# Kernel tuning notes

Measured on AMD Instinct MI355X. Metric: run time of the kernel, lower is better.

The kernel has to match this reference:

```python
import jax, jax.numpy as jnp
import numpy as np

B, T, S, D, VOCAB = 16, 64, 128, 512, 32000


def setup_inputs():
    key = jax.random.key(0)
    ks = jax.random.split(key, 20)
    w = lambda i, shape: jax.random.normal(ks[i], shape, dtype=jnp.float32) * 0.05
    return {
        'words': jax.random.randint(ks[0], (B, T), 0, VOCAB),
        'encoder_output': jax.random.normal(ks[1], (B, S, D), dtype=jnp.float32),
        'pre_h': jax.random.normal(ks[2], (B, D), dtype=jnp.float32),
        'cell': jax.random.normal(ks[3], (B, D), dtype=jnp.float32),
        'emb': w(4, (VOCAB, D)),
        'W_ih': w(5, (4 * D, D)), 'W_hh': w(6, (4 * D, D)),
        'b_ih': w(7, (4 * D,)), 'b_hh': w(8, (4 * D,)),
        'Wh_w': w(9, (D, D)),
        'Ws_w': w(10, (D, D)), 'Ws_b': w(11, (D,)),
        'vt_w': w(12, (D,)),
        'V_w': w(13, (D, 2 * D)), 'V_b': w(14, (D,)),
        'Vp_w': w(15, (VOCAB, D)), 'Vp_b': w(16, (VOCAB,)),
    }


def lstm(xs, h0, c0, W_ih, W_hh, b_ih, b_hh):
    # xs: [T, B, D]; PyTorch LSTM gate order: i, f, g, o
    def step(carry, x_t):
        h, c = carry
        g = x_t @ W_ih.T + b_ih + h @ W_hh.T + b_hh
        i, f, gg, o = jnp.split(g, 4, axis=-1)
        c = jax.nn.sigmoid(f) * c + jax.nn.sigmoid(i) * jnp.tanh(gg)
        h = jax.nn.sigmoid(o) * jnp.tanh(c)
        return (h, c), h
    _, hs = jax.lax.scan(step, (h0, c0), xs)
    return hs


def reference(words, encoder_output, pre_h, cell, emb, W_ih, W_hh, b_ih, b_hh,
              Wh_w, Ws_w, Ws_b, vt_w, V_w, V_b, Vp_w, Vp_b):
    x = emb[words]                                   # [B, T, D]
    hs = lstm(x.transpose(1, 0, 2), pre_h, cell, W_ih, W_hh, b_ih, b_hh)
    out = hs.transpose(1, 0, 2)                      # [B, T, D] decoder states
    wh = encoder_output @ Wh_w.T                     # [B, S, D]
    ws = out @ Ws_w.T + Ws_b                         # [B, T, D]
    # Bahdanau additive attention scores e[b,s,t] = v_t . tanh(wh[b,s] + ws[b,t])
    e = jnp.einsum('bstd,d->bst', jnp.tanh(wh[:, :, None, :] + ws[:, None, :, :]), vt_w)
    a = jax.nn.softmax(e, axis=1)                    # softmax over source positions
    context = jnp.einsum('bst,bsd->btd', a, encoder_output)
    cat = jnp.concatenate([context, out], axis=-1)   # [B, T, 2D]
    return (cat @ V_w.T + V_b) @ Vp_w.T + Vp_b       # [B, T, VOCAB]
```

## Files before the change

### kernel.cpp

```cpp
#include <hip/hip_runtime.h>

#define DEV __device__ __forceinline__

typedef float f32x4 __attribute__((ext_vector_type(4)));
typedef short s16x8 __attribute__((ext_vector_type(8)));
typedef unsigned short u16;
typedef u16 u16x4 __attribute__((ext_vector_type(4)));
typedef u16 u16x8 __attribute__((ext_vector_type(8)));
typedef unsigned int u32x4 __attribute__((ext_vector_type(4)));

constexpr int Bb = 16, Tt = 64, Ss = 128, Dd = 512, Vv = 32000, FD = 2048;

DEV u16 f2bf(float x) {
  unsigned u = __builtin_bit_cast(unsigned, x);
  u = u + 0x7fffu + ((u >> 16) & 1u);
  return (u16)(u >> 16);
}
DEV float bf2f(u16 h) { unsigned u = ((unsigned)h) << 16; return __builtin_bit_cast(float, u); }
DEV float sigm(float x) { return 1.f / (1.f + __expf(-x)); }
DEV float ftanh(float x) {
  x = fminf(15.f, fmaxf(-15.f, x));
  float e = __expf(2.f * x);
  return (e - 1.f) / (e + 1.f);
}

DEV void cvt_plain_one(const float* __restrict__ in, u16* __restrict__ out, int i) {
  float4 v = reinterpret_cast<const float4*>(in)[i];
  u16x4 o;
  o.x = f2bf(v.x); o.y = f2bf(v.y); o.z = f2bf(v.z); o.w = f2bf(v.w);
  reinterpret_cast<u16x4*>(out)[i] = o;
}

DEV void cvt_split_one(const float* __restrict__ in, u16* __restrict__ hi,
                       u16* __restrict__ lo, int i) {
  float4 v = reinterpret_cast<const float4*>(in)[i];
  u16x4 oh, ol;
  float vv[4] = {v.x, v.y, v.z, v.w};
#pragma unroll
  for (int j = 0; j < 4; ++j) {
    u16 h = f2bf(vv[j]);
    oh[j] = h;
    ol[j] = f2bf(vv[j] - bf2f(h));
  }
  reinterpret_cast<u16x4*>(hi)[i] = oh;
  reinterpret_cast<u16x4*>(lo)[i] = ol;
}

__global__ void k_cvt_pre(const float* __restrict__ Wih, u16* __restrict__ Wih_bf, int n0,
                          const float* __restrict__ enc, u16* __restrict__ ench,
                          u16* __restrict__ encl, int n1,
                          const float* __restrict__ Whw, u16* __restrict__ whh,
                          u16* __restrict__ whl, int n2) {
  int total = n0 + n1 + n2;
  int i = blockIdx.x * blockDim.x + threadIdx.x;
  int st = gridDim.x * blockDim.x;
  for (; i < total; i += st) {
    if (i < n0) cvt_plain_one(Wih, Wih_bf, i);
    else if (i < n0 + n1) cvt_split_one(enc, ench, encl, i - n0);
    else cvt_split_one(Whw, whh, whl, i - n0 - n1);
  }
}

__global__ void k_prep(const int* __restrict__ words, const float* __restrict__ emb,
                       u16* __restrict__ xb,
                       const float* __restrict__ pre, unsigned* __restrict__ hp0,
                       const float* __restrict__ bi, const float* __restrict__ bh,
                       float* __restrict__ bsum) {
  int blk = blockIdx.x, tid = threadIdx.x;
  if (blk < Bb * Tt) {
    int row = words[blk];
    int d = tid * 2;
    float2 v = *reinterpret_cast<const float2*>(&emb[(size_t)row * Dd + d]);
    xb[(size_t)blk * Dd + d] = f2bf(v.x);
    xb[(size_t)blk * Dd + d + 1] = f2bf(v.y);
  } else if (blk < Bb * Tt + 32) {
    int i = (blk - Bb * Tt) * 256 + tid;
    float v = pre[i];
    u16 h = f2bf(v);
    u16 l = f2bf(v - bf2f(h));
    hp0[i] = (unsigned)h | ((unsigned)l << 16);
  } else {
    int i = (blk - Bb * Tt - 32) * 256 + tid;
    bsum[i] = bi[i] + bh[i];
  }
}

template <bool BIAS, bool OUTBF, int TERMS>
DEV void gemm_body(u16* ls, int tile, int tid,
                   const u16* __restrict__ A, const u16* __restrict__ Al,
                   const u16* __restrict__ Bm, const u16* __restrict__ Bl,
                   float* __restrict__ Cf, u16* __restrict__ Cb,
                   const float* __restrict__ bias, int M, int N, int K) {
  u16* lsA = ls;
  u16* lsB = ls + 128 * 32;
  u16* lsAl = ls + 2 * 128 * 32;
  u16* lsBl = ls + 3 * 128 * 32;
  const int mt = M >> 7;
  const int tm = (tile % mt) << 7;
  const int tn = (tile / mt) << 7;
  const int wave = tid >> 6, lane = tid & 63;
  const int wr = wave >> 1, wc = wave & 1;
  f32x4 acc[4][4];
#pragma unroll
  for (int i = 0; i < 4; ++i)
#pragma unroll
    for (int j = 0; j < 4; ++j) acc[i][j] = (f32x4){0.f, 0.f, 0.f, 0.f};

  const int lrow = lane >> 2;
  const int lk = (lane & 3) << 3;
  const int fr = lane & 15, fk = (lane >> 4) << 3;

  for (int k0 = 0; k0 < K; k0 += 32) {
#pragma unroll
    for (int r = 0; r < 2; ++r) {
      int rowA = r * 64 + wave * 16;
      size_t goffA = (size_t)(tm + rowA + lrow) * K + k0 + lk;
      size_t goffB = (size_t)(tn + rowA + lrow) * K + k0 + lk;
      __builtin_amdgcn_global_load_lds((const __attribute__((address_space(1))) void*)(A + goffA),
                                       (__attribute__((address_space(3))) void*)&lsA[rowA * 32],
                                       16, 0, 0);
      __builtin_amdgcn_global_load_lds((const __attribute__((address_space(1))) void*)(Bm + goffB),
                                       (__attribute__((address_space(3))) void*)&lsB[rowA * 32],
                                       16, 0, 0);
      if constexpr (TERMS == 3) {
        __builtin_amdgcn_global_load_lds((const __attribute__((address_space(1))) void*)(Al + goffA),
                                         (__attribute__((address_space(3))) void*)&lsAl[rowA * 32],
                                         16, 0, 0);
        __builtin_amdgcn_global_load_lds((const __attribute__((address_space(1))) void*)(Bl + goffB),
                                         (__attribute__((address_space(3))) void*)&lsBl[rowA * 32],
                                         16, 0, 0);
      }
    }
    __syncthreads();
    s16x8 av[4], bv[4];
#pragma unroll
    for (int mi = 0; mi < 4; ++mi)
      av[mi] = *reinterpret_cast<const s16x8*>(&lsA[(wr * 64 + mi * 16 + fr) * 32 + fk]);
#pragma unroll
    for (int ni = 0; ni < 4; ++ni)
      bv[ni] = *reinterpret_cast<const s16x8*>(&lsB[(wc * 64 + ni * 16 + fr) * 32 + fk]);
    if constexpr (TERMS == 3) {
      s16x8 avl[4], bvl[4];
#pragma unroll
      for (int mi = 0; mi < 4; ++mi)
        avl[mi] = *reinterpret_cast<const s16x8*>(&lsAl[(wr * 64 + mi * 16 + fr) * 32 + fk]);
#pragma unroll
      for (int ni = 0; ni < 4; ++ni)
        bvl[ni] = *reinterpret_cast<const s16x8*>(&lsBl[(wc * 64 + ni * 16 + fr) * 32 + fk]);
#pragma unroll
      for (int mi = 0; mi < 4; ++mi)
#pragma unroll
        for (int ni = 0; ni < 4; ++ni) {
          acc[mi][ni] = __builtin_amdgcn_mfma_f32_16x16x32_bf16(av[mi], bv[ni], acc[mi][ni], 0, 0, 0);
          acc[mi][ni] = __builtin_amdgcn_mfma_f32_16x16x32_bf16(av[mi], bvl[ni], acc[mi][ni], 0, 0, 0);
          acc[mi][ni] = __builtin_amdgcn_mfma_f32_16x16x32_bf16(avl[mi], bv[ni], acc[mi][ni], 0, 0, 0);
        }
    } else {
#pragma unroll
      for (int mi = 0; mi < 4; ++mi)
#pragma unroll
        for (int ni = 0; ni < 4; ++ni)
          acc[mi][ni] = __builtin_amdgcn_mfma_f32_16x16x32_bf16(av[mi], bv[ni], acc[mi][ni], 0, 0, 0);
    }
    __syncthreads();
  }

  const int fm = (lane >> 4) << 2;
#pragma unroll
  for (int ni = 0; ni < 4; ++ni) {
    int col = tn + wc * 64 + ni * 16 + fr;
    float badd = 0.f;
    if constexpr (BIAS) badd = bias[col];
#pragma unroll
    for (int mi = 0; mi < 4; ++mi) {
#pragma unroll
      for (int r = 0; r < 4; ++r) {
        int row = tm + wr * 64 + mi * 16 + fm + r;
        size_t idx = (size_t)row * N + col;
        float v = acc[mi][ni][r] + badd;
        if constexpr (OUTBF) Cb[idx] = f2bf(v);
        else Cf[idx] = v;
      }
    }
  }
}

template <bool BIAS, bool OUTBF, int TERMS>
__global__ __launch_bounds__(256) void k_gemm(const u16* __restrict__ A,
                                              const u16* __restrict__ Al,
                                              const u16* __restrict__ Bm,
                                              const u16* __restrict__ Bl,
                                              float* __restrict__ Cf, u16* __restrict__ Cb,
                                              const float* __restrict__ bias,
                                              int M, int N, int K) {
  __shared__ u16 ls[4 * 128 * 32];
  gemm_body<BIAS, OUTBF, TERMS>(ls, blockIdx.x, threadIdx.x, A, Al, Bm, Bl, Cf, Cb, bias, M, N, K);
}

DEV void lstm_body(int w, int tid, float* gls,
                   const float* __restrict__ xg, const float* __restrict__ Whh,
                   const float* __restrict__ cell, unsigned* __restrict__ hpack,
                   u16* __restrict__ out_hi, u16* __restrict__ out_lo,
                   int* __restrict__ flags) {
  const int gi = tid >> 6, lane = tid & 63;
  const int ds0 = w << 4;
  float (*g_lds)[16][16] = (float(*)[16][16])gls;

  const int fr = lane & 15;
  const int fkb = (lane >> 4) << 3;

  s16x8 whi[16], wlo[16];
  {
    const float* wrow = Whh + (size_t)(gi * Dd + ds0 + fr) * Dd;
#pragma unroll
    for (int kc = 0; kc < 16; ++kc) {
      int k = kc * 32 + fkb;
      float4 a = *reinterpret_cast<const float4*>(&wrow[k]);
      float4 b = *reinterpret_cast<const float4*>(&wrow[k + 4]);
      float vv[8] = {a.x, a.y, a.z, a.w, b.x, b.y, b.z, b.w};
#pragma unroll
      for (int j = 0; j < 8; ++j) {
        u16 h = f2bf(vv[j]);
        whi[kc][j] = (short)h;
        wlo[kc][j] = (short)f2bf(vv[j] - bf2f(h));
      }
    }
  }

  const int ub = tid >> 4, ud = tid & 15;
  float c = cell[(size_t)ub * Dd + ds0 + ud];

  for (int t = 0; t < Tt; ++t) {
    float xgv[4];
#pragma unroll
    for (int r = 0; r < 4; ++r) {
      int bb = ((lane >> 4) << 2) + r;
      xgv[r] = xg[(size_t)(bb * Tt + t) * FD + gi * Dd + ds0 + fr];
    }
#pragma unroll
    for (int r = 0; r < 4; ++r) asm volatile("" ::"v"(xgv[r]));

    if (t > 0) {
      if (gi == 0) {
        if (lane < 32 && lane != w) {
          while (__hip_atomic_load(&flags[lane * 32], __ATOMIC_RELAXED,
                                   __HIP_MEMORY_SCOPE_AGENT) < t) {}
          while (__hip_atomic_load(&flags[lane * 32], __ATOMIC_ACQUIRE,
                                   __HIP_MEMORY_SCOPE_AGENT) < t) {}
        }
        __builtin_amdgcn_sched_barrier(0);
      }
      __syncthreads();
    }

    const unsigned* hp = hpack + (size_t)t * (Bb * Dd) + (size_t)fr * Dd;
    f32x4 a0 = (f32x4){0.f, 0.f, 0.f, 0.f};
    f32x4 a1 = a0, a2 = a0;
#pragma unroll
    for (int kc = 0; kc < 16; ++kc) {
      int k = kc * 32 + fkb;
      u32x4 u0 = *reinterpret_cast<const u32x4*>(&hp[k]);
      u32x4 u1 = *reinterpret_cast<const u32x4*>(&hp[k + 4]);
      s16x8 ahi, alo;
#pragma unroll
      for (int j = 0; j < 4; ++j) {
        ahi[j] = (short)(u0[j] & 0xffffu); alo[j] = (short)(u0[j] >> 16);
        ahi[4 + j] = (short)(u1[j] & 0xffffu); alo[4 + j] = (short)(u1[j] >> 16);
      }
      a0 = __builtin_amdgcn_mfma_f32_16x16x32_bf16(ahi, whi[kc], a0, 0, 0, 0);
      a1 = __builtin_amdgcn_mfma_f32_16x16x32_bf16(ahi, wlo[kc], a1, 0, 0, 0);
      a2 = __builtin_amdgcn_mfma_f32_16x16x32_bf16(alo, whi[kc], a2, 0, 0, 0);
    }
#pragma unroll
    for (int r = 0; r < 4; ++r) {
      int bb = ((lane >> 4) << 2) + r;
      g_lds[gi][bb][fr] = a0[r] + a1[r] + a2[r] + xgv[r];
    }
    __syncthreads();
    float iv = g_lds[0][ub][ud], fv = g_lds[1][ub][ud];
    float gv = g_lds[2][ub][ud], ov = g_lds[3][ub][ud];
    c = sigm(fv) * c + sigm(iv) * ftanh(gv);
    float h = sigm(ov) * ftanh(c);
    u16 hh = f2bf(h);
    u16 hl = f2bf(h - bf2f(hh));
    unsigned pk = (unsigned)hh | ((unsigned)hl << 16);
    __hip_atomic_store(&hpack[(size_t)(t + 1) * (Bb * Dd) + ub * Dd + ds0 + ud], pk,
                       __ATOMIC_RELAXED, __HIP_MEMORY_SCOPE_AGENT);
    size_t oidx = (size_t)(ub * Tt + t) * Dd + ds0 + ud;
    out_hi[oidx] = hh;
    out_lo[oidx] = hl;
    __syncthreads();
    if (tid == 0)
      __hip_atomic_store(&flags[w * 32], t + 1, __ATOMIC_RELAXED, __HIP_MEMORY_SCOPE_AGENT);
  }
}

__global__ __launch_bounds__(256) void k_lstm_fused(
    const float* __restrict__ xg, const float* __restrict__ Whh,
    const float* __restrict__ cell, unsigned* __restrict__ hpack,
    u16* __restrict__ out_hi, u16* __restrict__ out_lo, int* __restrict__ flags,
    const u16* __restrict__ enc_hi, const u16* __restrict__ enc_lo,
    const u16* __restrict__ Whw_hi, const u16* __restrict__ Whw_lo,
    float* __restrict__ wh,
    const float* __restrict__ Vp_w, u16* __restrict__ Vp_bf,
    const float* __restrict__ V_w, u16* __restrict__ Vw_bf,
    const float* __restrict__ Ws_w, u16* __restrict__ Wsw_hi, u16* __restrict__ Wsw_lo) {
  __shared__ u16 ls[4 * 128 * 32];
  const int blk = blockIdx.x, tid = threadIdx.x;
  if (blk < 32) {
    lstm_body(blk, tid, (float*)ls, xg, Whh, cell, hpack, out_hi, out_lo, flags);
  } else if (blk < 96) {
    gemm_body<false, false, 3>(ls, blk - 32, tid, enc_hi, enc_lo, Whw_hi, Whw_lo,
                               wh, nullptr, nullptr, 2048, 512, 512);
  } else {
    const int nVp = Vv * Dd / 4, nV = Dd * 2 * Dd / 4, nWs = Dd * Dd / 4;
    int total = nVp + nV + nWs;
    int i = (blk - 96) * 256 + tid;
    int st = 160 * 256;
    for (; i < total; i += st) {
      if (i < nVp) cvt_plain_one(Vp_w, Vp_bf, i);
      else if (i < nVp + nV) cvt_plain_one(V_w, Vw_bf, i - nVp);
      else cvt_split_one(Ws_w, Wsw_hi, Wsw_lo, i - nVp - nV);
    }
  }
}

__global__ __launch_bounds__(256) void k_attn(const float* __restrict__ wh,
                                              const float* __restrict__ wst,
                                              const float* __restrict__ vt,
                                              const float* __restrict__ enc,
                                              const u16* __restrict__ out_hi,
                                              u16* __restrict__ cat) {
  const int tid = threadIdx.x;
  const int wave = tid >> 6, lane = tid & 63;
  const int wid = blockIdx.x * 4 + wave;
  const int b = wid >> 6, t = wid & 63;
  const int d0 = lane << 3;

  float wsv[8], vtv[8];
  {
    const float4* p = reinterpret_cast<const float4*>(&wst[(size_t)(b * Tt + t) * Dd + d0]);
    float4 x = p[0], y = p[1];
    wsv[0] = x.x; wsv[1] = x.y; wsv[2] = x.z; wsv[3] = x.w;
    wsv[4] = y.x; wsv[5] = y.y; wsv[6] = y.z; wsv[7] = y.w;
    const float4* q = reinterpret_cast<const float4*>(&vt[d0]);
    float4 u = q[0], v = q[1];
    vtv[0] = u.x; vtv[1] = u.y; vtv[2] = u.z; vtv[3] = u.w;
    vtv[4] = v.x; vtv[5] = v.y; vtv[6] = v.z; vtv[7] = v.w;
  }
  float e0 = 0.f, e1 = 0.f;
  for (int s = 0; s < Ss; ++s) {
    const float4* p = reinterpret_cast<const float4*>(&wh[(size_t)(b * Ss + s) * Dd + d0]);
    float4 x = p[0], y = p[1];
    float whv[8] = {x.x, x.y, x.z, x.w, y.x, y.y, y.z, y.w};
    float a = 0.f;
#pragma unroll
    for (int j = 0; j < 8; ++j) a += ftanh(whv[j] + wsv[j]) * vtv[j];
#pragma unroll
    for (int off = 32; off; off >>= 1) a += __shfl_xor(a, off);
    if (lane == (s & 63)) { if (s < 64) e0 = a; else e1 = a; }
  }
  float m = fmaxf(e0, e1);
#pragma unroll
  for (int off = 32; off; off >>= 1) m = fmaxf(m, __shfl_xor(m, off));
  float p0 = __expf(e0 - m), p1 = __expf(e1 - m);
  float sum = p0 + p1;
#pragma unroll
  for (int off = 32; off; off >>= 1) sum += __shfl_xor(sum, off);
  float inv = 1.f / sum;
  float a0 = p0 * inv, a1 = p1 * inv;

  float ctx[8] = {0.f, 0.f, 0.f, 0.f, 0.f, 0.f, 0.f, 0.f};
  for (int s = 0; s < Ss; ++s) {
    float as = __shfl(s < 64 ? a0 : a1, s & 63);
    const float4* p = reinterpret_cast<const float4*>(&enc[(size_t)(b * Ss + s) * Dd + d0]);
    float4 x = p[0], y = p[1];
    ctx[0] += as * x.x; ctx[1] += as * x.y; ctx[2] += as * x.z; ctx[3] += as * x.w;
    ctx[4] += as * y.x; ctx[5] += as * y.y; ctx[6] += as * y.z; ctx[7] += as * y.w;
  }
  u16x8 co;
#pragma unroll
  for (int j = 0; j < 8; ++j) co[j] = f2bf(ctx[j]);
  size_t cbase = (size_t)(b * Tt + t) * (2 * Dd);
  *reinterpret_cast<u16x8*>(&cat[cbase + d0]) = co;
  u16x8 ov = *reinterpret_cast<const u16x8*>(&out_hi[(size_t)(b * Tt + t) * Dd + d0]);
  *reinterpret_cast<u16x8*>(&cat[cbase + Dd + d0]) = ov;
}

extern "C" void kernel_launch(void* const* d_in, const int* in_sizes, int n_in,
                              void* d_out, int out_size, void* d_ws, size_t ws_size,
                              hipStream_t stream) {
  const int* words = (const int*)d_in[0];
  const float* enc = (const float*)d_in[1];
  const float* pre_h = (const float*)d_in[2];
  const float* cell = (const float*)d_in[3];
  const float* emb = (const float*)d_in[4];
  const float* W_ih = (const float*)d_in[5];
  const float* W_hh = (const float*)d_in[6];
  const float* b_ih = (const float*)d_in[7];
  const float* b_hh = (const float*)d_in[8];
  const float* Wh_w = (const float*)d_in[9];
  const float* Ws_w = (const float*)d_in[10];
  const float* Ws_b = (const float*)d_in[11];
  const float* vt_w = (const float*)d_in[12];
  const float* V_w = (const float*)d_in[13];
  const float* V_b = (const float*)d_in[14];
  const float* Vp_w = (const float*)d_in[15];
  const float* Vp_b = (const float*)d_in[16];
  float* outp = (float*)d_out;

  char* ws = (char*)d_ws;
  size_t off = 0;
  auto alloc = [&](size_t bytes) {
    char* p = ws + off;
    off = (off + bytes + 255) & ~(size_t)255;
    return p;
  };
  int* flags = (int*)alloc(4096);
  float* xg = (float*)alloc((size_t)Bb * Tt * FD * 4);
  float* wh = (float*)alloc((size_t)Bb * Ss * Dd * 4);
  float* wst = (float*)alloc((size_t)Bb * Tt * Dd * 4);
  unsigned* hpack = (unsigned*)alloc((size_t)(Tt + 1) * Bb * Dd * 4);
  u16* out_hi = (u16*)alloc((size_t)Bb * Tt * Dd * 2);
  u16* out_lo = (u16*)alloc((size_t)Bb * Tt * Dd * 2);
  u16* x_bf = (u16*)alloc((size_t)Bb * Tt * Dd * 2);
  u16* enc_hi = (u16*)alloc((size_t)Bb * Ss * Dd * 2);
  u16* enc_lo = (u16*)alloc((size_t)Bb * Ss * Dd * 2);
  u16* Wih_bf = (u16*)alloc((size_t)FD * Dd * 2);
  u16* Whw_hi = (u16*)alloc((size_t)Dd * Dd * 2);
  u16* Whw_lo = (u16*)alloc((size_t)Dd * Dd * 2);
  u16* Wsw_hi = (u16*)alloc((size_t)Dd * Dd * 2);
  u16* Wsw_lo = (u16*)alloc((size_t)Dd * Dd * 2);
  u16* Vw_bf = (u16*)alloc((size_t)Dd * 2 * Dd * 2);
  u16* Vp_bf = (u16*)alloc((size_t)Vv * Dd * 2);
  u16* cat = (u16*)alloc((size_t)Bb * Tt * 2 * Dd * 2);
  u16* hmid = (u16*)alloc((size_t)Bb * Tt * Dd * 2);
  float* bsum = (float*)alloc((size_t)FD * 4);
  if (off > ws_size) return;

  hipMemsetAsync(flags, 0, 4096, stream);

  k_cvt_pre<<<256, 256, 0, stream>>>(W_ih, Wih_bf, FD * Dd / 4,
                                     enc, enc_hi, enc_lo, Bb * Ss * Dd / 4,
                                     Wh_w, Whw_hi, Whw_lo, Dd * Dd / 4);
  k_prep<<<Bb * Tt + 32 + 8, 256, 0, stream>>>(words, emb, x_bf, pre_h, (unsigned*)hpack,
                                               b_ih, b_hh, bsum);
  k_gemm<true, false, 1><<<8 * 16, 256, 0, stream>>>(x_bf, nullptr, Wih_bf, nullptr,
                                                     xg, nullptr, bsum, 1024, 2048, 512);
  k_lstm_fused<<<256, 256, 0, stream>>>(xg, W_hh, cell, (unsigned*)hpack, out_hi, out_lo,
                                        flags, enc_hi, enc_lo, Whw_hi, Whw_lo, wh,
                                        Vp_w, Vp_bf, V_w, Vw_bf, Ws_w, Wsw_hi, Wsw_lo);
  k_gemm<true, false, 3><<<8 * 4, 256, 0, stream>>>(out_hi, out_lo, Wsw_hi, Wsw_lo,
                                                    wst, nullptr, Ws_b, 1024, 512, 512);
  k_attn<<<256, 256, 0, stream>>>(wh, wst, vt_w, enc, out_hi, cat);
  k_gemm<true, true, 1><<<8 * 4, 256, 0, stream>>>(cat, nullptr, Vw_bf, nullptr,
                                                   nullptr, hmid, V_b, 1024, 512, 1024);
  k_gemm<true, false, 1><<<8 * 250, 256, 0, stream>>>(hmid, nullptr, Vp_bf, nullptr,
                                                      outp, nullptr, Vp_b, 1024, 32000, 512);
}
```

Before: 592.0 us.

## Replace LSTM flag barrier with sentinel-polled hidden-state loads

Drops the per-step cross-block flag spin-wait and __syncthreads in the persistent LSTM. Instead, hpack slots for steps 1..T are pre-filled with a sentinel pattern, and each wave issues all 32 hidden-state loads up front with cache-bypassing asm. It then re-polls any vector that still holds the sentinel until the data arrives. This removes a global-flag round trip and barrier from the serial recurrence critical path, but adds 512 sentinel-fill blocks and relies on per-word store visibility and on the sentinel never matching a real packed hi/lo value.

```diff
diff --git a/kernel.cpp b/kernel.cpp
--- a/kernel.cpp
+++ b/kernel.cpp
@@ -10,6 +10,7 @@
 typedef unsigned int u32x4 __attribute__((ext_vector_type(4)));
 
 constexpr int Bb = 16, Tt = 64, Ss = 128, Dd = 512, Vv = 32000, FD = 2048;
+constexpr unsigned SENT = 0x7FFF7FFFu;
 
 DEV u16 f2bf(float x) {
   unsigned u = __builtin_bit_cast(unsigned, x);
@@ -22,6 +23,21 @@
   x = fminf(15.f, fmaxf(-15.f, x));
   float e = __expf(2.f * x);
   return (e - 1.f) / (e + 1.f);
+}
+
+template <int OFF>
+DEV u32x4 issue_load(const unsigned* p) {
+  u32x4 v;
+  asm volatile("global_load_dwordx4 %0, %1, off offset:%2 sc0 sc1"
+               : "=v"(v) : "v"(p), "n"(OFF) : "memory");
+  return v;
+}
+template <int OFF>
+DEV u32x4 reload_sync(const unsigned* p) {
+  u32x4 v;
+  asm volatile("global_load_dwordx4 %0, %1, off offset:%2 sc0 sc1\n\ts_waitcnt vmcnt(0)"
+               : "=v"(v) : "v"(p), "n"(OFF) : "memory");
+  return v;
 }
 
 DEV void cvt_plain_one(const float* __restrict__ in, u16* __restrict__ out, int i) {
@@ -79,9 +95,12 @@
     u16 h = f2bf(v);
     u16 l = f2bf(v - bf2f(h));
     hp0[i] = (unsigned)h | ((unsigned)l << 16);
-  } else {
+  } else if (blk < Bb * Tt + 32 + 8) {
     int i = (blk - Bb * Tt - 32) * 256 + tid;
     bsum[i] = bi[i] + bh[i];
+  } else {
+    int i = (blk - (Bb * Tt + 40)) * 256 + tid;
+    reinterpret_cast<u32x4*>(hp0 + Bb * Dd)[i] = (u32x4){SENT, SENT, SENT, SENT};
   }
 }
 
@@ -197,11 +216,21 @@
   gemm_body<BIAS, OUTBF, TERMS>(ls, blockIdx.x, threadIdx.x, A, Al, Bm, Bl, Cf, Cb, bias, M, N, K);
 }
 
+#define OFFC(c) (((c) >> 1) * 128 + ((c)&1) * 16)
+#define ISSUE(c) hbuf[c] = issue_load<OFFC(c)>(hpl)
+#define CHECK(c)                                                           \
+  {                                                                        \
+    u32x4 v = hbuf[c];                                                     \
+    if (v[0] == SENT || v[1] == SENT || v[2] == SENT || v[3] == SENT) {    \
+      hbuf[c] = reload_sync<OFFC(c)>(hpl);                                 \
+      bad = 1u;                                                            \
+    }                                                                      \
+  }
+
 DEV void lstm_body(int w, int tid, float* gls,
                    const float* __restrict__ xg, const float* __restrict__ Whh,
                    const float* __restrict__ cell, unsigned* __restrict__ hpack,
-                   u16* __restrict__ out_hi, u16* __restrict__ out_lo,
-                   int* __restrict__ flags) {
+                   u16* __restrict__ out_hi, u16* __restrict__ out_lo) {
   const int gi = tid >> 6, lane = tid & 63;
   const int ds0 = w << 4;
   float (*g_lds)[16][16] = (float(*)[16][16])gls;
@@ -237,30 +266,31 @@
       int bb = ((lane >> 4) << 2) + r;
       xgv[r] = xg[(size_t)(bb * Tt + t) * FD + gi * Dd + ds0 + fr];
     }
-#pragma unroll
-    for (int r = 0; r < 4; ++r) asm volatile("" ::"v"(xgv[r]));
-
-    if (t > 0) {
-      if (gi == 0) {
-        if (lane < 32 && lane != w) {
-          while (__hip_atomic_load(&flags[lane * 32], __ATOMIC_RELAXED,
-                                   __HIP_MEMORY_SCOPE_AGENT) < t) {}
-          while (__hip_atomic_load(&flags[lane * 32], __ATOMIC_ACQUIRE,
-                                   __HIP_MEMORY_SCOPE_AGENT) < t) {}
-        }
-        __builtin_amdgcn_sched_barrier(0);
-      }
-      __syncthreads();
-    }
-
-    const unsigned* hp = hpack + (size_t)t * (Bb * Dd) + (size_t)fr * Dd;
+
+    const unsigned* hpl = hpack + (size_t)t * (Bb * Dd) + (size_t)fr * Dd + fkb;
+    u32x4 hbuf[32];
+    ISSUE(0);  ISSUE(1);  ISSUE(2);  ISSUE(3);  ISSUE(4);  ISSUE(5);  ISSUE(6);  ISSUE(7);
+    ISSUE(8);  ISSUE(9);  ISSUE(10); ISSUE(11); ISSUE(12); ISSUE(13); ISSUE(14); ISSUE(15);
+    ISSUE(16); ISSUE(17); ISSUE(18); ISSUE(19); ISSUE(20); ISSUE(21); ISSUE(22); ISSUE(23);
+    ISSUE(24); ISSUE(25); ISSUE(26); ISSUE(27); ISSUE(28); ISSUE(29); ISSUE(30); ISSUE(31);
+    asm volatile("s_waitcnt vmcnt(0)" ::: "memory");
+    __builtin_amdgcn_sched_barrier(0);
+    for (;;) {
+      unsigned bad = 0;
+      CHECK(0);  CHECK(1);  CHECK(2);  CHECK(3);  CHECK(4);  CHECK(5);  CHECK(6);  CHECK(7);
+      CHECK(8);  CHECK(9);  CHECK(10); CHECK(11); CHECK(12); CHECK(13); CHECK(14); CHECK(15);
+      CHECK(16); CHECK(17); CHECK(18); CHECK(19); CHECK(20); CHECK(21); CHECK(22); CHECK(23);
+      CHECK(24); CHECK(25); CHECK(26); CHECK(27); CHECK(28); CHECK(29); CHECK(30); CHECK(31);
+      if (!__any(bad)) break;
+    }
+    __builtin_amdgcn_sched_barrier(0);
+
     f32x4 a0 = (f32x4){0.f, 0.f, 0.f, 0.f};
     f32x4 a1 = a0, a2 = a0;
 #pragma unroll
     for (int kc = 0; kc < 16; ++kc) {
-      int k = kc * 32 + fkb;
-      u32x4 u0 = *reinterpret_cast<const u32x4*>(&hp[k]);
-      u32x4 u1 = *reinterpret_cast<const u32x4*>(&hp[k + 4]);
+      u32x4 u0 = hbuf[2 * kc];
+      u32x4 u1 = hbuf[2 * kc + 1];
       s16x8 ahi, alo;
 #pragma unroll
       for (int j = 0; j < 4; ++j) {
@@ -290,15 +320,13 @@
     out_hi[oidx] = hh;
     out_lo[oidx] = hl;
     __syncthreads();
-    if (tid == 0)
-      __hip_atomic_store(&flags[w * 32], t + 1, __ATOMIC_RELAXED, __HIP_MEMORY_SCOPE_AGENT);
-  }
-}
-
-__global__ __launch_bounds__(256) void k_lstm_fused(
+  }
+}
+
+__global__ __launch_bounds__(256, 1) void k_lstm_fused(
     const float* __restrict__ xg, const float* __restrict__ Whh,
     const float* __restrict__ cell, unsigned* __restrict__ hpack,
-    u16* __restrict__ out_hi, u16* __restrict__ out_lo, int* __restrict__ flags,
+    u16* __restrict__ out_hi, u16* __restrict__ out_lo,
     const u16* __restrict__ enc_hi, const u16* __restrict__ enc_lo,
     const u16* __restrict__ Whw_hi, const u16* __restrict__ Whw_lo,
     float* __restrict__ wh,
@@ -308,7 +336,7 @@
   __shared__ u16 ls[4 * 128 * 32];
   const int blk = blockIdx.x, tid = threadIdx.x;
   if (blk < 32) {
-    lstm_body(blk, tid, (float*)ls, xg, Whh, cell, hpack, out_hi, out_lo, flags);
+    lstm_body(blk, tid, (float*)ls, xg, Whh, cell, hpack, out_hi, out_lo);
   } else if (blk < 96) {
     gemm_body<false, false, 3>(ls, blk - 32, tid, enc_hi, enc_lo, Whw_hi, Whw_lo,
                                wh, nullptr, nullptr, 2048, 512, 512);
@@ -416,7 +444,6 @@
     off = (off + bytes + 255) & ~(size_t)255;
     return p;
   };
-  int* flags = (int*)alloc(4096);
   float* xg = (float*)alloc((size_t)Bb * Tt * FD * 4);
   float* wh = (float*)alloc((size_t)Bb * Ss * Dd * 4);
   float* wst = (float*)alloc((size_t)Bb * Tt * Dd * 4);
@@ -438,17 +465,15 @@
   float* bsum = (float*)alloc((size_t)FD * 4);
   if (off > ws_size) return;
 
-  hipMemsetAsync(flags, 0, 4096, stream);
-
   k_cvt_pre<<<256, 256, 0, stream>>>(W_ih, Wih_bf, FD * Dd / 4,
                                      enc, enc_hi, enc_lo, Bb * Ss * Dd / 4,
                                      Wh_w, Whw_hi, Whw_lo, Dd * Dd / 4);
-  k_prep<<<Bb * Tt + 32 + 8, 256, 0, stream>>>(words, emb, x_bf, pre_h, (unsigned*)hpack,
-                                               b_ih, b_hh, bsum);
+  k_prep<<<Bb * Tt + 32 + 8 + 512, 256, 0, stream>>>(words, emb, x_bf, pre_h,
+                                                     (unsigned*)hpack, b_ih, b_hh, bsum);
   k_gemm<true, false, 1><<<8 * 16, 256, 0, stream>>>(x_bf, nullptr, Wih_bf, nullptr,
                                                      xg, nullptr, bsum, 1024, 2048, 512);
   k_lstm_fused<<<256, 256, 0, stream>>>(xg, W_hh, cell, (unsigned*)hpack, out_hi, out_lo,
-                                        flags, enc_hi, enc_lo, Whw_hi, Whw_lo, wh,
+                                        enc_hi, enc_lo, Whw_hi, Whw_lo, wh,
                                         Vp_w, Vp_bf, V_w, Vw_bf, Ws_w, Wsw_hi, Wsw_lo);
   k_gemm<true, false, 3><<<8 * 4, 256, 0, stream>>>(out_hi, out_lo, Wsw_hi, Wsw_lo,
                                                     wst, nullptr, Ws_b, 1024, 512, 512);
```

New measurement: 785.5 us. 1.33x slower.

## Fuse LSTM, attention tail and logits into one flag-synchronized megakernel

Applied to the files above, without the earlier changes.

Replaces the separate Ws GEMM, attention, V GEMM and vocabulary GEMM launches with one persistent kernel. Roles are split by block index: LSTM blocks, Wh GEMM blocks, weight-conversion blocks, per-time-chunk tail blocks (Ws projection, attention, V projection) and logits blocks. Blocks are coordinated through global counters, so attention and logits for earlier time chunks can run while the LSTM recurrence is still going. The decoder-state layout changes to time-major to suit this chunking. In exchange it relies on all 506 blocks being co-resident, since spin-waits would deadlock otherwise. It also adds cache-bypassing stores, and the logits path keeps a leftover dead prologue loop.

```diff
diff --git a/kernel.cpp b/kernel.cpp
--- a/kernel.cpp
+++ b/kernel.cpp
@@ -17,6 +17,7 @@
   return (u16)(u >> 16);
 }
 DEV float bf2f(u16 h) { unsigned u = ((unsigned)h) << 16; return __builtin_bit_cast(float, u); }
+DEV unsigned pack2(float a, float b) { return (unsigned)f2bf(a) | ((unsigned)f2bf(b) << 16); }
 DEV float sigm(float x) { return 1.f / (1.f + __expf(-x)); }
 DEV float ftanh(float x) {
   x = fminf(15.f, fmaxf(-15.f, x));
@@ -24,13 +25,35 @@
   return (e - 1.f) / (e + 1.f);
 }
 
+DEV void st_short_sc(u16* p, u16 v) {
+  asm volatile("global_store_short %0, %1, off sc0 sc1" ::"v"(p), "v"((unsigned)v) : "memory");
+}
+DEV void st_dword_sc(float* p, float v) {
+  asm volatile("global_store_dword %0, %1, off sc0 sc1" ::"v"(p), "v"(v) : "memory");
+}
+DEV void st_dwordu_sc(unsigned* p, unsigned v) {
+  asm volatile("global_store_dword %0, %1, off sc0 sc1" ::"v"(p), "v"(v) : "memory");
+}
+#define VM0 asm volatile("s_waitcnt vmcnt(0)" ::: "memory")
+
+DEV int ld_rel(const int* p) {
+  return __hip_atomic_load(p, __ATOMIC_RELAXED, __HIP_MEMORY_SCOPE_AGENT);
+}
+DEV int ld_acq(const int* p) {
+  return __hip_atomic_load(p, __ATOMIC_ACQUIRE, __HIP_MEMORY_SCOPE_AGENT);
+}
+DEV void ctr_inc(int* p) {
+  __hip_atomic_fetch_add(p, 1, __ATOMIC_RELAXED, __HIP_MEMORY_SCOPE_AGENT);
+}
+
+constexpr int CTRL_WH = 1024, CTRL_CVT = 1056, CTRL_HM = 1088;
+
 DEV void cvt_plain_one(const float* __restrict__ in, u16* __restrict__ out, int i) {
   float4 v = reinterpret_cast<const float4*>(in)[i];
   u16x4 o;
   o.x = f2bf(v.x); o.y = f2bf(v.y); o.z = f2bf(v.z); o.w = f2bf(v.w);
   reinterpret_cast<u16x4*>(out)[i] = o;
 }
-
 DEV void cvt_split_one(const float* __restrict__ in, u16* __restrict__ hi,
                        u16* __restrict__ lo, int i) {
   float4 v = reinterpret_cast<const float4*>(in)[i];
@@ -85,12 +108,12 @@
   }
 }
 
-template <bool BIAS, bool OUTBF, int TERMS>
+template <bool BIAS, int TERMS, int CST>
 DEV void gemm_body(u16* ls, int tile, int tid,
                    const u16* __restrict__ A, const u16* __restrict__ Al,
                    const u16* __restrict__ Bm, const u16* __restrict__ Bl,
-                   float* __restrict__ Cf, u16* __restrict__ Cb,
-                   const float* __restrict__ bias, int M, int N, int K) {
+                   float* __restrict__ Cf, const float* __restrict__ bias,
+                   int M, int N, int K) {
   u16* lsA = ls;
   u16* lsB = ls + 128 * 32;
   u16* lsAl = ls + 2 * 128 * 32;
@@ -178,30 +201,31 @@
         int row = tm + wr * 64 + mi * 16 + fm + r;
         size_t idx = (size_t)row * N + col;
         float v = acc[mi][ni][r] + badd;
-        if constexpr (OUTBF) Cb[idx] = f2bf(v);
+        if constexpr (CST == 2) st_dword_sc(&Cf[idx], v);
         else Cf[idx] = v;
       }
     }
   }
-}
-
-template <bool BIAS, bool OUTBF, int TERMS>
+  if constexpr (CST == 2) VM0;
+}
+
+template <bool BIAS, int TERMS>
 __global__ __launch_bounds__(256) void k_gemm(const u16* __restrict__ A,
                                               const u16* __restrict__ Al,
                                               const u16* __restrict__ Bm,
                                               const u16* __restrict__ Bl,
-                                              float* __restrict__ Cf, u16* __restrict__ Cb,
+                                              float* __restrict__ Cf,
                                               const float* __restrict__ bias,
                                               int M, int N, int K) {
   __shared__ u16 ls[4 * 128 * 32];
-  gemm_body<BIAS, OUTBF, TERMS>(ls, blockIdx.x, threadIdx.x, A, Al, Bm, Bl, Cf, Cb, bias, M, N, K);
+  gemm_body<BIAS, TERMS, 0>(ls, blockIdx.x, threadIdx.x, A, Al, Bm, Bl, Cf, bias, M, N, K);
 }
 
 DEV void lstm_body(int w, int tid, float* gls,
                    const float* __restrict__ xg, const float* __restrict__ Whh,
                    const float* __restrict__ cell, unsigned* __restrict__ hpack,
                    u16* __restrict__ out_hi, u16* __restrict__ out_lo,
-                   int* __restrict__ flags) {
+                   int* __restrict__ ctrl) {
   const int gi = tid >> 6, lane = tid & 63;
   const int ds0 = w << 4;
   float (*g_lds)[16][16] = (float(*)[16][16])gls;
@@ -243,10 +267,8 @@
     if (t > 0) {
       if (gi == 0) {
         if (lane < 32 && lane != w) {
-          while (__hip_atomic_load(&flags[lane * 32], __ATOMIC_RELAXED,
-                                   __HIP_MEMORY_SCOPE_AGENT) < t) {}
-          while (__hip_atomic_load(&flags[lane * 32], __ATOMIC_ACQUIRE,
-                                   __HIP_MEMORY_SCOPE_AGENT) < t) {}
+          while (ld_rel(&ctrl[lane * 32]) < t) {}
+          while (ld_acq(&ctrl[lane * 32]) < t) {}
         }
         __builtin_amdgcn_sched_barrier(0);
       }
@@ -286,105 +308,332 @@
     unsigned pk = (unsigned)hh | ((unsigned)hl << 16);
     __hip_atomic_store(&hpack[(size_t)(t + 1) * (Bb * Dd) + ub * Dd + ds0 + ud], pk,
                        __ATOMIC_RELAXED, __HIP_MEMORY_SCOPE_AGENT);
-    size_t oidx = (size_t)(ub * Tt + t) * Dd + ds0 + ud;
-    out_hi[oidx] = hh;
-    out_lo[oidx] = hl;
+    size_t oidx = (size_t)(t * Bb + ub) * Dd + ds0 + ud;
+    st_short_sc(&out_hi[oidx], hh);
+    st_short_sc(&out_lo[oidx], hl);
+    VM0;
     __syncthreads();
     if (tid == 0)
-      __hip_atomic_store(&flags[w * 32], t + 1, __ATOMIC_RELAXED, __HIP_MEMORY_SCOPE_AGENT);
-  }
-}
-
-__global__ __launch_bounds__(256) void k_lstm_fused(
+      __hip_atomic_store(&ctrl[w * 32], t + 1, __ATOMIC_RELAXED, __HIP_MEMORY_SCOPE_AGENT);
+  }
+}
+
+DEV void tail_body(int c, int b, int tid, u16* ls,
+                   const u16* __restrict__ out_hi, const u16* __restrict__ out_lo,
+                   const u16* __restrict__ Wsw_hi, const u16* __restrict__ Wsw_lo,
+                   const float* __restrict__ Ws_b,
+                   const float* __restrict__ wh, const float* __restrict__ vt,
+                   const float* __restrict__ enc,
+                   const u16* __restrict__ Vw_bf, const float* __restrict__ V_b,
+                   u16* __restrict__ hmid, int* __restrict__ ctrl) {
+  const int wv = tid >> 6, lane = tid & 63;
+  const int fr = lane & 15, fkb = (lane >> 4) << 3;
+  float (*ws_s)[Dd] = (float(*)[Dd])ls;
+  u16 (*cat_s)[2 * Dd] = (u16(*)[2 * Dd])(ls + 8192);
+
+  if (wv == 0) {
+    int tgt = (c + 1) * 8;
+    if (lane < 32) {
+      while (ld_rel(&ctrl[lane * 32]) < tgt) __builtin_amdgcn_s_sleep(2);
+    } else if (lane == 32) {
+      while (ld_rel(&ctrl[CTRL_WH]) < 64) __builtin_amdgcn_s_sleep(2);
+    } else if (lane == 33) {
+      while (ld_rel(&ctrl[CTRL_CVT]) < 32) __builtin_amdgcn_s_sleep(2);
+    }
+    __builtin_amdgcn_sched_barrier(0);
+    if (lane == 0) {
+      while (ld_acq(&ctrl[CTRL_CVT]) < 32) {}
+    }
+    __builtin_amdgcn_sched_barrier(0);
+  }
+  __syncthreads();
+
+  {
+    f32x4 acc8[8];
+#pragma unroll
+    for (int n = 0; n < 8; ++n) acc8[n] = (f32x4){0.f, 0.f, 0.f, 0.f};
+    const int j = fr & 7;
+    const size_t arow = ((size_t)(c * 8 + j) * Bb + b) * Dd;
+    for (int kc = 0; kc < 16; ++kc) {
+      int k = kc * 32 + fkb;
+      s16x8 ah = *reinterpret_cast<const s16x8*>(&out_hi[arow + k]);
+      s16x8 al = *reinterpret_cast<const s16x8*>(&out_lo[arow + k]);
+#pragma unroll
+      for (int n = 0; n < 8; ++n) {
+        size_t brow = (size_t)(wv * 128 + n * 16 + fr) * Dd + k;
+        s16x8 bh = *reinterpret_cast<const s16x8*>(&Wsw_hi[brow]);
+        s16x8 bl = *reinterpret_cast<const s16x8*>(&Wsw_lo[brow]);
+        acc8[n] = __builtin_amdgcn_mfma_f32_16x16x32_bf16(ah, bh, acc8[n], 0, 0, 0);
+        acc8[n] = __builtin_amdgcn_mfma_f32_16x16x32_bf16(ah, bl, acc8[n], 0, 0, 0);
+        acc8[n] = __builtin_amdgcn_mfma_f32_16x16x32_bf16(al, bh, acc8[n], 0, 0, 0);
+      }
+    }
+#pragma unroll
+    for (int n = 0; n < 8; ++n) {
+      int col = wv * 128 + n * 16 + fr;
+      float badd = Ws_b[col];
+#pragma unroll
+      for (int r = 0; r < 4; ++r) {
+        int row = (lane >> 4) * 4 + r;
+        if (row < 8) ws_s[row][col] = acc8[n][r] + badd;
+      }
+    }
+  }
+  __syncthreads();
+
+  {
+    const int d0 = lane << 3;
+    float vtv[8];
+    {
+      const float4* q = reinterpret_cast<const float4*>(&vt[d0]);
+      float4 u = q[0], v = q[1];
+      vtv[0] = u.x; vtv[1] = u.y; vtv[2] = u.z; vtv[3] = u.w;
+      vtv[4] = v.x; vtv[5] = v.y; vtv[6] = v.z; vtv[7] = v.w;
+    }
+    for (int rr = 0; rr < 2; ++rr) {
+      int j = wv * 2 + rr;
+      float wsv[8];
+#pragma unroll
+      for (int d = 0; d < 8; ++d) wsv[d] = ws_s[j][d0 + d];
+      float e0 = 0.f, e1 = 0.f;
+      for (int s = 0; s < Ss; ++s) {
+        const float4* p = reinterpret_cast<const float4*>(&wh[(size_t)(b * Ss + s) * Dd + d0]);
+        float4 x = p[0], y = p[1];
+        float whv[8] = {x.x, x.y, x.z, x.w, y.x, y.y, y.z, y.w};
+        float a = 0.f;
+#pragma unroll
+        for (int d = 0; d < 8; ++d) a += ftanh(whv[d] + wsv[d]) * vtv[d];
+#pragma unroll
+        for (int off = 32; off; off >>= 1) a += __shfl_xor(a, off);
+        if (lane == (s & 63)) { if (s < 64) e0 = a; else e1 = a; }
+      }
+      float m = fmaxf(e0, e1);
+#pragma unroll
+      for (int off = 32; off; off >>= 1) m = fmaxf(m, __shfl_xor(m, off));
+      float p0 = __expf(e0 - m), p1 = __expf(e1 - m);
+      float sum = p0 + p1;
+#pragma unroll
+      for (int off = 32; off; off >>= 1) sum += __shfl_xor(sum, off);
+      float inv = 1.f / sum;
+      float a0s = p0 * inv, a1s = p1 * inv;
+      float ctx[8] = {0.f, 0.f, 0.f, 0.f, 0.f, 0.f, 0.f, 0.f};
+      for (int s = 0; s < Ss; ++s) {
+        float as = __shfl(s < 64 ? a0s : a1s, s & 63);
+        const float4* p = reinterpret_cast<const float4*>(&enc[(size_t)(b * Ss + s) * Dd + d0]);
+        float4 x = p[0], y = p[1];
+        ctx[0] += as * x.x; ctx[1] += as * x.y; ctx[2] += as * x.z; ctx[3] += as * x.w;
+        ctx[4] += as * y.x; ctx[5] += as * y.y; ctx[6] += as * y.z; ctx[7] += as * y.w;
+      }
+      u16x8 co;
+#pragma unroll
+      for (int d = 0; d < 8; ++d) co[d] = f2bf(ctx[d]);
+      *reinterpret_cast<u16x8*>(&cat_s[j][d0]) = co;
+      size_t orow = ((size_t)(c * 8 + j) * Bb + b) * Dd;
+      u16x8 ov = *reinterpret_cast<const u16x8*>(&out_hi[orow + d0]);
+      *reinterpret_cast<u16x8*>(&cat_s[j][Dd + d0]) = ov;
+    }
+  }
+  __syncthreads();
+
+  {
+    f32x4 acc8[8];
+#pragma unroll
+    for (int n = 0; n < 8; ++n) acc8[n] = (f32x4){0.f, 0.f, 0.f, 0.f};
+    const int j = fr & 7;
+    for (int kc = 0; kc < 32; ++kc) {
+      int k = kc * 32 + fkb;
+      s16x8 a = *reinterpret_cast<const s16x8*>(&cat_s[j][k]);
+#pragma unroll
+      for (int n = 0; n < 8; ++n) {
+        size_t brow = (size_t)(wv * 128 + n * 16 + fr) * (2 * Dd) + k;
+        s16x8 bf = *reinterpret_cast<const s16x8*>(&Vw_bf[brow]);
+        acc8[n] = __builtin_amdgcn_mfma_f32_16x16x32_bf16(a, bf, acc8[n], 0, 0, 0);
+      }
+    }
+#pragma unroll
+    for (int n = 0; n < 8; ++n) {
+      int col = wv * 128 + n * 16 + fr;
+      float badd = V_b[col];
+#pragma unroll
+      for (int r = 0; r < 4; ++r) {
+        int row = (lane >> 4) * 4 + r;
+        if (row < 8) {
+          size_t grow = ((size_t)(c * 8 + row) * Bb + b) * Dd + col;
+          st_short_sc(&hmid[grow], f2bf(acc8[n][r] + badd));
+        }
+      }
+    }
+  }
+  VM0;
+  __syncthreads();
+  if (tid == 0) ctr_inc(&ctrl[CTRL_HM + 32 * c]);
+}
+
+DEV void logits_body(int n, int tid, u16* ls,
+                     const u16* __restrict__ hmid, const u16* __restrict__ Vp_bf,
+                     const float* __restrict__ Vp_b, float* __restrict__ out,
+                     int* __restrict__ ctrl) {
+  u16* lsA = ls;
+  u16* lsB = ls + 128 * 32;
+  const int wave = tid >> 6, lane = tid & 63;
+  const int wr = wave >> 1, wc = wave & 1;
+  const int lrow = lane >> 2, lk = (lane & 3) << 3;
+  const int fr = lane & 15, fk = (lane >> 4) << 3;
+  const int fm = (lane >> 4) << 2;
+
+  if (wave == 0) {
+    if (lane == 0) {
+      while (ld_rel(&ctrl[CTRL_CVT]) < 32) __builtin_amdgcn_s_sleep(2);
+      while (ld_acq(&ctrl[CTRL_CVT]) < 32) {}
+    }
+    __builtin_amdgcn_sched_barrier(0);
+  }
+  __syncthreads();
+
+  for (int c = 0; c < 8; ++c) {
+    if (wave == 0 && lane == 0) {
+      while (ld_rel(&ctrl[CTRL_HM + 32 * c]) < 16) __builtin_amdgcn_s_sleep(2);
+      while (ld_acq(&ctrl[CTRL_HM + 32 * c]) < 16) {}
+    }
+    __syncthreads();
+
+    f32x4 acc[4];
+#pragma unroll
+    for (int i = 0; i < 4; ++i) acc[i] = (f32x4){0.f, 0.f, 0.f, 0.f};
+    for (int k0 = 0; k0 < 512; k0 += 32) {
+#pragma unroll
+      for (int r = 0; r < 2; ++r) {
+        int rowA = r * 64 + wave * 16;
+        size_t goffA = (size_t)(c * 128 + rowA + lrow) * 512 + k0 + lk;
+        size_t goffB = (size_t)(n * 128 + rowA + lrow) * 512 + k0 + lk;
+        __builtin_amdgcn_global_load_lds(
+            (const __attribute__((address_space(1))) void*)(hmid + goffA),
+            (__attribute__((address_space(3))) void*)&lsA[rowA * 32], 16, 0, 0);
+        __builtin_amdgcn_global_load_lds(
+            (const __attribute__((address_space(1))) void*)(Vp_bf + goffB),
+            (__attribute__((address_space(3))) void*)&lsB[rowA * 32], 16, 0, 0);
+      }
+      __syncthreads();
+      s16x8 av[4], bv[4];
+#pragma unroll
+      for (int mi = 0; mi < 4; ++mi)
+        av[mi] = *reinterpret_cast<const s16x8*>(&lsA[(wr * 64 + mi * 16 + fr) * 32 + fk]);
+#pragma unroll
+      for (int ni = 0; ni < 4; ++ni)
+        bv[ni] = *reinterpret_cast<const s16x8*>(&lsB[(wc * 64 + ni * 16 + fr) * 32 + fk]);
+#pragma unroll
+      for (int mi = 0; mi < 4; ++mi) {
+      }
+      static_assert(true, "");
+      (void)av; (void)bv;
+      __syncthreads();
+      break;
+    }
+    f32x4 accq[4][4];
+#pragma unroll
+    for (int i = 0; i < 4; ++i)
+#pragma unroll
+      for (int j2 = 0; j2 < 4; ++j2) accq[i][j2] = (f32x4){0.f, 0.f, 0.f, 0.f};
+    for (int k0 = 0; k0 < 512; k0 += 32) {
+#pragma unroll
+      for (int r = 0; r < 2; ++r) {
+        int rowA = r * 64 + wave * 16;
+        size_t goffA = (size_t)(c * 128 + rowA + lrow) * 512 + k0 + lk;
+        size_t goffB = (size_t)(n * 128 + rowA + lrow) * 512 + k0 + lk;
+        __builtin_amdgcn_global_load_lds(
+            (const __attribute__((address_space(1))) void*)(hmid + goffA),
+            (__attribute__((address_space(3))) void*)&lsA[rowA * 32], 16, 0, 0);
+        __builtin_amdgcn_global_load_lds(
+            (const __attribute__((address_space(1))) void*)(Vp_bf + goffB),
+            (__attribute__((address_space(3))) void*)&lsB[rowA * 32], 16, 0, 0);
+      }
+      __syncthreads();
+      s16x8 av[4], bv[4];
+#pragma unroll
+      for (int mi = 0; mi < 4; ++mi)
+        av[mi] = *reinterpret_cast<const s16x8*>(&lsA[(wr * 64 + mi * 16 + fr) * 32 + fk]);
+#pragma unroll
+      for (int ni = 0; ni < 4; ++ni)
+        bv[ni] = *reinterpret_cast<const s16x8*>(&lsB[(wc * 64 + ni * 16 + fr) * 32 + fk]);
+#pragma unroll
+      for (int mi = 0; mi < 4; ++mi)
+#pragma unroll
+        for (int ni = 0; ni < 4; ++ni)
+          accq[mi][ni] = __builtin_amdgcn_mfma_f32_16x16x32_bf16(av[mi], bv[ni], accq[mi][ni], 0, 0, 0);
+      __syncthreads();
+    }
+#pragma unroll
+    for (int ni = 0; ni < 4; ++ni) {
+      int col = n * 128 + wc * 64 + ni * 16 + fr;
+      float badd = Vp_b[col];
+#pragma unroll
+      for (int mi = 0; mi < 4; ++mi) {
+#pragma unroll
+        for (int r = 0; r < 4; ++r) {
+          int rowl = wr * 64 + mi * 16 + fm + r;
+          int grow = c * 128 + rowl;
+          int tt = grow >> 4, bi = grow & 15;
+          out[((size_t)bi * Tt + tt) * Vv + col] = accq[mi][ni][r] + badd;
+        }
+      }
+    }
+  }
+}
+
+__global__ __launch_bounds__(256) void k_mega(
     const float* __restrict__ xg, const float* __restrict__ Whh,
     const float* __restrict__ cell, unsigned* __restrict__ hpack,
-    u16* __restrict__ out_hi, u16* __restrict__ out_lo, int* __restrict__ flags,
+    u16* __restrict__ out_hi, u16* __restrict__ out_lo, int* __restrict__ ctrl,
     const u16* __restrict__ enc_hi, const u16* __restrict__ enc_lo,
     const u16* __restrict__ Whw_hi, const u16* __restrict__ Whw_lo,
     float* __restrict__ wh,
     const float* __restrict__ Vp_w, u16* __restrict__ Vp_bf,
     const float* __restrict__ V_w, u16* __restrict__ Vw_bf,
-    const float* __restrict__ Ws_w, u16* __restrict__ Wsw_hi, u16* __restrict__ Wsw_lo) {
+    const float* __restrict__ Ws_w, u16* __restrict__ Wsw_hi, u16* __restrict__ Wsw_lo,
+    const float* __restrict__ Ws_b, const float* __restrict__ vt,
+    const float* __restrict__ enc, const float* __restrict__ V_b,
+    u16* __restrict__ hmid, const float* __restrict__ Vp_b, float* __restrict__ outp) {
   __shared__ u16 ls[4 * 128 * 32];
   const int blk = blockIdx.x, tid = threadIdx.x;
   if (blk < 32) {
-    lstm_body(blk, tid, (float*)ls, xg, Whh, cell, hpack, out_hi, out_lo, flags);
+    lstm_body(blk, tid, (float*)ls, xg, Whh, cell, hpack, out_hi, out_lo, ctrl);
   } else if (blk < 96) {
-    gemm_body<false, false, 3>(ls, blk - 32, tid, enc_hi, enc_lo, Whw_hi, Whw_lo,
-                               wh, nullptr, nullptr, 2048, 512, 512);
+    gemm_body<false, 3, 2>(ls, blk - 32, tid, enc_hi, enc_lo, Whw_hi, Whw_lo,
+                           wh, nullptr, 2048, 512, 512);
+    __syncthreads();
+    if (tid == 0) ctr_inc(&ctrl[CTRL_WH]);
+  } else if (blk < 128) {
+    const int nVpP = Vv * Dd / 2, nVwP = Dd * 2 * Dd / 2, nWsP = Dd * Dd / 2;
+    int total = nVpP + nVwP + nWsP;
+    int i = (blk - 96) * 256 + tid;
+    int st = 32 * 256;
+    for (; i < total; i += st) {
+      if (i < nVpP) {
+        float2 v = reinterpret_cast<const float2*>(Vp_w)[i];
+        st_dwordu_sc(&reinterpret_cast<unsigned*>(Vp_bf)[i], pack2(v.x, v.y));
+      } else if (i < nVpP + nVwP) {
+        int j = i - nVpP;
+        float2 v = reinterpret_cast<const float2*>(V_w)[j];
+        st_dwordu_sc(&reinterpret_cast<unsigned*>(Vw_bf)[j], pack2(v.x, v.y));
+      } else {
+        int j = i - nVpP - nVwP;
+        float2 v = reinterpret_cast<const float2*>(Ws_w)[j];
+        u16 h0 = f2bf(v.x), h1 = f2bf(v.y);
+        u16 l0 = f2bf(v.x - bf2f(h0)), l1 = f2bf(v.y - bf2f(h1));
+        st_dwordu_sc(&reinterpret_cast<unsigned*>(Wsw_hi)[j], (unsigned)h0 | ((unsigned)h1 << 16));
+        st_dwordu_sc(&reinterpret_cast<unsigned*>(Wsw_lo)[j], (unsigned)l0 | ((unsigned)l1 << 16));
+      }
+    }
+    VM0;
+    __syncthreads();
+    if (tid == 0) ctr_inc(&ctrl[CTRL_CVT]);
+  } else if (blk < 256) {
+    int c = (blk - 128) >> 4, b = (blk - 128) & 15;
+    tail_body(c, b, tid, ls, out_hi, out_lo, Wsw_hi, Wsw_lo, Ws_b, wh, vt, enc,
+              Vw_bf, V_b, hmid, ctrl);
   } else {
-    const int nVp = Vv * Dd / 4, nV = Dd * 2 * Dd / 4, nWs = Dd * Dd / 4;
-    int total = nVp + nV + nWs;
-    int i = (blk - 96) * 256 + tid;
-    int st = 160 * 256;
-    for (; i < total; i += st) {
-      if (i < nVp) cvt_plain_one(Vp_w, Vp_bf, i);
-      else if (i < nVp + nV) cvt_plain_one(V_w, Vw_bf, i - nVp);
-      else cvt_split_one(Ws_w, Wsw_hi, Wsw_lo, i - nVp - nV);
-    }
-  }
-}
-
-__global__ __launch_bounds__(256) void k_attn(const float* __restrict__ wh,
-                                              const float* __restrict__ wst,
-                                              const float* __restrict__ vt,
-                                              const float* __restrict__ enc,
-                                              const u16* __restrict__ out_hi,
-                                              u16* __restrict__ cat) {
-  const int tid = threadIdx.x;
-  const int wave = tid >> 6, lane = tid & 63;
-  const int wid = blockIdx.x * 4 + wave;
-  const int b = wid >> 6, t = wid & 63;
-  const int d0 = lane << 3;
-
-  float wsv[8], vtv[8];
-  {
-    const float4* p = reinterpret_cast<const float4*>(&wst[(size_t)(b * Tt + t) * Dd + d0]);
-    float4 x = p[0], y = p[1];
-    wsv[0] = x.x; wsv[1] = x.y; wsv[2] = x.z; wsv[3] = x.w;
-    wsv[4] = y.x; wsv[5] = y.y; wsv[6] = y.z; wsv[7] = y.w;
-    const float4* q = reinterpret_cast<const float4*>(&vt[d0]);
-    float4 u = q[0], v = q[1];
-    vtv[0] = u.x; vtv[1] = u.y; vtv[2] = u.z; vtv[3] = u.w;
-    vtv[4] = v.x; vtv[5] = v.y; vtv[6] = v.z; vtv[7] = v.w;
-  }
-  float e0 = 0.f, e1 = 0.f;
-  for (int s = 0; s < Ss; ++s) {
-    const float4* p = reinterpret_cast<const float4*>(&wh[(size_t)(b * Ss + s) * Dd + d0]);
-    float4 x = p[0], y = p[1];
-    float whv[8] = {x.x, x.y, x.z, x.w, y.x, y.y, y.z, y.w};
-    float a = 0.f;
-#pragma unroll
-    for (int j = 0; j < 8; ++j) a += ftanh(whv[j] + wsv[j]) * vtv[j];
-#pragma unroll
-    for (int off = 32; off; off >>= 1) a += __shfl_xor(a, off);
-    if (lane == (s & 63)) { if (s < 64) e0 = a; else e1 = a; }
-  }
-  float m = fmaxf(e0, e1);
-#pragma unroll
-  for (int off = 32; off; off >>= 1) m = fmaxf(m, __shfl_xor(m, off));
-  float p0 = __expf(e0 - m), p1 = __expf(e1 - m);
-  float sum = p0 + p1;
-#pragma unroll
-  for (int off = 32; off; off >>= 1) sum += __shfl_xor(sum, off);
-  float inv = 1.f / sum;
-  float a0 = p0 * inv, a1 = p1 * inv;
-
-  float ctx[8] = {0.f, 0.f, 0.f, 0.f, 0.f, 0.f, 0.f, 0.f};
-  for (int s = 0; s < Ss; ++s) {
-    float as = __shfl(s < 64 ? a0 : a1, s & 63);
-    const float4* p = reinterpret_cast<const float4*>(&enc[(size_t)(b * Ss + s) * Dd + d0]);
-    float4 x = p[0], y = p[1];
-    ctx[0] += as * x.x; ctx[1] += as * x.y; ctx[2] += as * x.z; ctx[3] += as * x.w;
-    ctx[4] += as * y.x; ctx[5] += as * y.y; ctx[6] += as * y.z; ctx[7] += as * y.w;
-  }
-  u16x8 co;
-#pragma unroll
-  for (int j = 0; j < 8; ++j) co[j] = f2bf(ctx[j]);
-  size_t cbase = (size_t)(b * Tt + t) * (2 * Dd);
-  *reinterpret_cast<u16x8*>(&cat[cbase + d0]) = co;
-  u16x8 ov = *reinterpret_cast<const u16x8*>(&out_hi[(size_t)(b * Tt + t) * Dd + d0]);
-  *reinterpret_cast<u16x8*>(&cat[cbase + Dd + d0]) = ov;
+    logits_body(blk - 256, tid, ls, hmid, Vp_bf, Vp_b, outp, ctrl);
+  }
 }
 
 extern "C" void kernel_launch(void* const* d_in, const int* in_sizes, int n_in,
@@ -416,10 +665,9 @@
     off = (off + bytes + 255) & ~(size_t)255;
     return p;
   };
-  int* flags = (int*)alloc(4096);
+  int* ctrl = (int*)alloc(8192);
   float* xg = (float*)alloc((size_t)Bb * Tt * FD * 4);
   float* wh = (float*)alloc((size_t)Bb * Ss * Dd * 4);
-  float* wst = (float*)alloc((size_t)Bb * Tt * Dd * 4);
   unsigned* hpack = (unsigned*)alloc((size_t)(Tt + 1) * Bb * Dd * 4);
   u16* out_hi = (u16*)alloc((size_t)Bb * Tt * Dd * 2);
   u16* out_lo = (u16*)alloc((size_t)Bb * Tt * Dd * 2);
@@ -433,28 +681,21 @@
   u16* Wsw_lo = (u16*)alloc((size_t)Dd * Dd * 2);
   u16* Vw_bf = (u16*)alloc((size_t)Dd * 2 * Dd * 2);
   u16* Vp_bf = (u16*)alloc((size_t)Vv * Dd * 2);
-  u16* cat = (u16*)alloc((size_t)Bb * Tt * 2 * Dd * 2);
   u16* hmid = (u16*)alloc((size_t)Bb * Tt * Dd * 2);
   float* bsum = (float*)alloc((size_t)FD * 4);
   if (off > ws_size) return;
 
-  hipMemsetAsync(flags, 0, 4096, stream);
+  hipMemsetAsync(ctrl, 0, 8192, stream);
 
   k_cvt_pre<<<256, 256, 0, stream>>>(W_ih, Wih_bf, FD * Dd / 4,
                                      enc, enc_hi, enc_lo, Bb * Ss * Dd / 4,
                                      Wh_w, Whw_hi, Whw_lo, Dd * Dd / 4);
-  k_prep<<<Bb * Tt + 32 + 8, 256, 0, stream>>>(words, emb, x_bf, pre_h, (unsigned*)hpack,
-                                               b_ih, b_hh, bsum);
-  k_gemm<true, false, 1><<<8 * 16, 256, 0, stream>>>(x_bf, nullptr, Wih_bf, nullptr,
-                                                     xg, nullptr, bsum, 1024, 2048, 512);
-  k_lstm_fused<<<256, 256, 0, stream>>>(xg, W_hh, cell, (unsigned*)hpack, out_hi, out_lo,
-                                        flags, enc_hi, enc_lo, Whw_hi, Whw_lo, wh,
-                                        Vp_w, Vp_bf, V_w, Vw_bf, Ws_w, Wsw_hi, Wsw_lo);
-  k_gemm<true, false, 3><<<8 * 4, 256, 0, stream>>>(out_hi, out_lo, Wsw_hi, Wsw_lo,
-                                                    wst, nullptr, Ws_b, 1024, 512, 512);
-  k_attn<<<256, 256, 0, stream>>>(wh, wst, vt_w, enc, out_hi, cat);
-  k_gemm<true, true, 1><<<8 * 4, 256, 0, stream>>>(cat, nullptr, Vw_bf, nullptr,
-                                                   nullptr, hmid, V_b, 1024, 512, 1024);
-  k_gemm<true, false, 1><<<8 * 250, 256, 0, stream>>>(hmid, nullptr, Vp_bf, nullptr,
-                                                      outp, nullptr, Vp_b, 1024, 32000, 512);
-}
+  k_prep<<<Bb * Tt + 32 + 8, 256, 0, stream>>>(words, emb, x_bf, pre_h,
+                                               (unsigned*)hpack, b_ih, b_hh, bsum);
+  k_gemm<true, 1><<<8 * 16, 256, 0, stream>>>(x_bf, nullptr, Wih_bf, nullptr,
+                                              xg, bsum, 1024, 2048, 512);
+  k_mega<<<506, 256, 0, stream>>>(xg, W_hh, cell, (unsigned*)hpack, out_hi, out_lo, ctrl,
+                                  enc_hi, enc_lo, Whw_hi, Whw_lo, wh,
+                                  Vp_w, Vp_bf, V_w, Vw_bf, Ws_w, Wsw_hi, Wsw_lo,
+                                  Ws_b, vt_w, enc, V_b, hmid, Vp_b, outp);
+}
```

After: 837.1 us. 41.4% more time.
